# Performance work log

Hardware: AMD Instinct MI355X
Metric: run time of the kernel (lower is better)

Reference implementation:

```python
import jax, jax.numpy as jnp
from jax import lax
import numpy as np

B, T, D_IN = 4, 1024, 8
D_MODEL, N_LAYERS, HORIZON, D_OUT = 512, 2, 24, 8
D_STATE, D_CONV, EXPAND = 64, 4, 2
D_INNER = EXPAND * D_MODEL
DT_RANK = -(-D_MODEL // 16)  # ceil(d_model/16) = 32
LN_EPS = 1e-5


def setup_inputs() -> dict:
    key = jax.random.key(0)
    ks = iter(jax.random.split(key, 24))
    rn = lambda shape, s: jax.random.normal(next(ks), shape, jnp.float32) * s
    A_log = jnp.tile(jnp.log(jnp.arange(1, D_STATE + 1, dtype=jnp.float32)), (N_LAYERS, D_INNER, 1))
    return {
        "x": rn((B, T, D_IN), 1.0),
        "W_in": rn((D_IN, D_MODEL), 0.3), "b_in": jnp.zeros((D_MODEL,), jnp.float32),
        "W_xz": rn((N_LAYERS, D_MODEL, 2 * D_INNER), 0.04),
        "conv_w": rn((N_LAYERS, D_INNER, D_CONV), 0.3), "conv_b": jnp.zeros((N_LAYERS, D_INNER), jnp.float32),
        "W_xproj": rn((N_LAYERS, D_INNER, DT_RANK + 2 * D_STATE), 0.03),
        "W_dt": rn((N_LAYERS, DT_RANK, D_INNER), 0.1), "b_dt": rn((N_LAYERS, D_INNER), 0.1) - 4.0,
        "A_log": A_log, "D_skip": jnp.ones((N_LAYERS, D_INNER), jnp.float32),
        "W_out": rn((N_LAYERS, D_INNER, D_MODEL), 0.03),
        "ln_g": jnp.ones((D_MODEL,), jnp.float32), "ln_b": jnp.zeros((D_MODEL,), jnp.float32),
        "W_h1": rn((D_MODEL, D_MODEL), 0.04), "b_h1": jnp.zeros((D_MODEL,), jnp.float32),
        "W_h2": rn((D_MODEL, HORIZON * D_OUT), 0.04), "b_h2": jnp.zeros((HORIZON * D_OUT,), jnp.float32),
    }


def mamba_block(h, Wxz, cw, cb, Wxp, Wdt, bdt, Alog, Dsk, Wout):
    # h: [B,T,d_model] -> [B,T,d_model]  (mamba-ssm Mamba block, no residual)
    xz = h @ Wxz                                   # [B,T,2*d_inner]
    xb, z = jnp.split(xz, 2, axis=-1)
    # depthwise causal conv over time
    xc = jnp.transpose(xb, (0, 2, 1))              # [B,d_inner,T]
    xc = lax.conv_general_dilated(xc, cw[:, None, :], (1,), [(D_CONV - 1, 0)],
                                  feature_group_count=D_INNER)
    xc = jax.nn.silu(xc + cb[None, :, None])
    xc = jnp.transpose(xc, (0, 2, 1))              # [B,T,d_inner]
    # input-dependent dt, B, C
    xdb = xc @ Wxp                                 # [B,T,dt_rank+2*d_state]
    dt_r = xdb[..., :DT_RANK]
    Bc = xdb[..., DT_RANK:DT_RANK + D_STATE]
    Cc = xdb[..., DT_RANK + D_STATE:]
    dt = jax.nn.softplus(dt_r @ Wdt + bdt)         # [B,T,d_inner]
    A = -jnp.exp(Alog)                             # [d_inner,d_state]

    def step(hst, ins):
        dt_t, B_t, C_t, x_t = ins                  # [B,d_inner],[B,N],[B,N],[B,d_inner]
        dA = jnp.exp(dt_t[..., None] * A)          # [B,d_inner,N]
        hst = dA * hst + dt_t[..., None] * B_t[:, None, :] * x_t[..., None]
        y = jnp.einsum('bdn,bn->bd', hst, C_t)
        return hst, y

    h0 = jnp.zeros((h.shape[0], D_INNER, D_STATE), h.dtype)
    xs = (jnp.transpose(dt, (1, 0, 2)), jnp.transpose(Bc, (1, 0, 2)),
          jnp.transpose(Cc, (1, 0, 2)), jnp.transpose(xc, (1, 0, 2)))
    _, ys = lax.scan(step, h0, xs)                 # ys: [T,B,d_inner]
    y = jnp.transpose(ys, (1, 0, 2)) + Dsk * xc
    y = y * jax.nn.silu(z)
    return y @ Wout


def reference(x, W_in, b_in, W_xz, conv_w, conv_b, W_xproj, W_dt, b_dt, A_log, D_skip,
              W_out, ln_g, ln_b, W_h1, b_h1, W_h2, b_h2):
    h = x @ W_in + b_in                            # [B,T,d_model]
    for i in range(N_LAYERS):
        h = mamba_block(h, W_xz[i], conv_w[i], conv_b[i], W_xproj[i], W_dt[i],
                        b_dt[i], A_log[i], D_skip[i], W_out[i])
    mu = jnp.mean(h, axis=-1, keepdims=True)
    var = jnp.mean(jnp.square(h - mu), axis=-1, keepdims=True)
    h = (h - mu) * lax.rsqrt(var + LN_EPS) * ln_g + ln_b
    last = h[:, -1, :]                             # [B,d_model]
    hid = jax.nn.gelu(last @ W_h1 + b_h1, approximate=False)
    yhat = hid @ W_h2 + b_h2                       # [B,horizon*d_out]
    return yhat.reshape(x.shape[0], HORIZON, D_OUT)
```

## Files before the change

### kernel.cpp

```cpp
#include <hip/hip_runtime.h>
#include <hip/hip_bf16.h>

static constexpr int kB      = 4;
static constexpr int kT      = 1024;
static constexpr int kDIN    = 8;
static constexpr int kDMODEL = 512;
static constexpr int kNLAYER = 2;
static constexpr int kHOR    = 24;
static constexpr int kDOUT   = 8;
static constexpr int kDSTATE = 64;
static constexpr int kDINNER = 1024;
static constexpr int kDTRANK = 32;
static constexpr int kXPROJ  = 160;
static constexpr int kXPAD   = 256;
static constexpr int kBT     = kB * kT;

typedef __bf16 bf16x8 __attribute__((ext_vector_type(8)));
typedef float  f32x4  __attribute__((ext_vector_type(4)));

__device__ __forceinline__ float silu_f(float x)     { return x / (1.f + __expf(-x)); }
__device__ __forceinline__ float softplus_f(float x) { return (x > 20.f) ? x : log1pf(__expf(x)); }
__device__ __forceinline__ float gelu_f(float x)     { return 0.5f * x * (1.f + erff(x * 0.70710678118654752f)); }

__device__ __forceinline__ void gld_lds16(const void* g, void* l) {
    __builtin_amdgcn_global_load_lds(
        (const __attribute__((address_space(1))) unsigned int*)g,
        (__attribute__((address_space(3))) unsigned int*)l, 16, 0, 0);
}

template<int CTRL>
__device__ __forceinline__ float dpp_mov(float v) {
    return __int_as_float(__builtin_amdgcn_update_dpp(
        0, __float_as_int(v), CTRL, 0xf, 0xf, false));
}

__global__ __launch_bounds__(256) void wtrans_kernel(
    const float* __restrict__ in, int K, int N, int in_lstride,
    __hip_bfloat16* __restrict__ out, int Kpad, int out_lstride)
{
    __shared__ float tile[32][33];
    const int tid = threadIdx.x;
    const int n0 = blockIdx.x * 32;
    const int k0 = blockIdx.y * 32;
    const float* inl = in + (size_t)blockIdx.z * in_lstride;
    __hip_bfloat16* outl = out + (size_t)blockIdx.z * out_lstride;

#pragma unroll
    for (int p = 0; p < 4; ++p) {
        int idx = p * 256 + tid;
        int ki = idx >> 5, ni = idx & 31;
        float v = 0.f;
        if (k0 + ki < K && n0 + ni < N) v = inl[(size_t)(k0 + ki) * N + n0 + ni];
        tile[ki][ni] = v;
    }
    __syncthreads();
#pragma unroll
    for (int p = 0; p < 4; ++p) {
        int idx = p * 256 + tid;
        int ni = idx >> 5, ki = idx & 31;
        outl[(size_t)(n0 + ni) * Kpad + k0 + ki] = __float2bfloat16(tile[ki][ni]);
    }
}

template<int MODE, int BN>
__global__ __launch_bounds__(256) void mfma_gemm_bt(
    const __hip_bfloat16* __restrict__ A, int lda,
    const __hip_bfloat16* __restrict__ BT, int ldb,
    const float* __restrict__ bias,
    float* __restrict__ C, int ldc,
    void* __restrict__ C2,
    int K)
{
    __shared__ __align__(16) __hip_bfloat16 sA[128][64];
    __shared__ __align__(16) __hip_bfloat16 sB[BN][64];

    const int tid  = threadIdx.x;
    const int lane = tid & 63;
    const int w    = tid >> 6;
    const int m0   = blockIdx.y * 128;
    const int n0   = blockIdx.x * BN;

    constexpr int NI = 4;
    constexpr int NJ = (BN == 128) ? 4 : 4;
    constexpr int MI = (BN == 128) ? 4 : 2;

    const int wm = (BN == 128) ? (w >> 1) : w;
    const int wn = (BN == 128) ? (w & 1) : 0;
    const int wmrows = (BN == 128) ? 64 : 32;

    f32x4 acc[MI][NJ] = {};

    const int lrow = lane & 15;
    const int lk   = (lane >> 4) << 3;

    const int grow = tid >> 3;
    const int gcol = (tid & 7) * 8;
    char* ldsA = (char*)&sA[0][0] + w * 1024;
    char* ldsB = (char*)&sB[0][0] + w * 1024;

    for (int k0 = 0; k0 < K; k0 += 64) {
        __syncthreads();
#pragma unroll
        for (int p = 0; p < 4; ++p)
            gld_lds16(A + (size_t)(m0 + grow + p * 32) * lda + k0 + gcol, ldsA + p * 4096);
#pragma unroll
        for (int p = 0; p < BN / 32; ++p)
            gld_lds16(BT + (size_t)(n0 + grow + p * 32) * ldb + k0 + gcol, ldsB + p * 4096);
        __syncthreads();
#pragma unroll
        for (int ks = 0; ks < 2; ++ks) {
            bf16x8 af[MI], bfr[NJ];
#pragma unroll
            for (int i = 0; i < MI; ++i)
                af[i] = *reinterpret_cast<const bf16x8*>(&sA[wm * wmrows + i * 16 + lrow][ks * 32 + lk]);
#pragma unroll
            for (int j = 0; j < NJ; ++j)
                bfr[j] = *reinterpret_cast<const bf16x8*>(&sB[wn * 64 + j * 16 + lrow][ks * 32 + lk]);
#pragma unroll
            for (int i = 0; i < MI; ++i)
#pragma unroll
                for (int j = 0; j < NJ; ++j)
                    acc[i][j] = __builtin_amdgcn_mfma_f32_16x16x32_bf16(af[i], bfr[j], acc[i][j], 0, 0, 0);
        }
    }

    const int crow = (lane >> 4) * 4;
    const int ccol = lane & 15;
#pragma unroll
    for (int i = 0; i < MI; ++i) {
#pragma unroll
        for (int j = 0; j < NJ; ++j) {
#pragma unroll
            for (int r = 0; r < 4; ++r) {
                int row = m0 + wm * wmrows + i * 16 + crow + r;
                int col = n0 + wn * 64 + j * 16 + ccol;
                float v = acc[i][j][r];
                if (MODE == 1) {
                    C[(size_t)row * ldc + col] = v;
                    ((__hip_bfloat16*)C2)[(size_t)row * ldc + col] = __float2bfloat16(v);
                } else if (MODE == 2) {
                    float dtv = softplus_f(v + bias[col]);
                    float xcv = __bfloat162float(((const __hip_bfloat16*)C2)[(size_t)row * kDINNER + col]);
                    size_t base = (size_t)(row >> 1) * 4096 + col * 4 + (row & 1) * 2;
                    C[base]     = dtv;
                    C[base + 1] = dtv * xcv;
                } else if (MODE == 4) {
                    if (col < kDINNER)
                        ((__hip_bfloat16*)C)[(size_t)row * ldc + col] = __float2bfloat16(v);
                    else
                        ((__hip_bfloat16*)C2)[(size_t)row * ldc + (col - kDINNER)] =
                            __float2bfloat16(silu_f(v));
                } else {
                    if (col < kDTRANK)
                        ((__hip_bfloat16*)C2)[(size_t)row * kXPAD + col] = __float2bfloat16(v);
                    else if (col < kDTRANK + kDSTATE)
                        C[(size_t)(row >> 1) * 256 + (col - kDTRANK) * 4 + (row & 1) * 2] = v;
                    else if (col < kXPROJ)
                        C[(size_t)(row >> 1) * 256 + (col - kDTRANK - kDSTATE) * 4 + (row & 1) * 2 + 1] = v;
                }
            }
        }
    }
}

__global__ __launch_bounds__(256) void in_proj_kernel(
    const float* __restrict__ x, const float* __restrict__ W,
    const float* __restrict__ b,
    float* __restrict__ h, __hip_bfloat16* __restrict__ hb)
{
    int idx = blockIdx.x * 256 + threadIdx.x;
    int n4 = (idx & 127) * 4;
    int m  = idx >> 7;
    float4 acc = *reinterpret_cast<const float4*>(b + n4);
    const float* xr = x + m * kDIN;
#pragma unroll
    for (int k = 0; k < kDIN; ++k) {
        float4 wv = *reinterpret_cast<const float4*>(W + k * kDMODEL + n4);
        float xv = xr[k];
        acc.x = fmaf(xv, wv.x, acc.x);
        acc.y = fmaf(xv, wv.y, acc.y);
        acc.z = fmaf(xv, wv.z, acc.z);
        acc.w = fmaf(xv, wv.w, acc.w);
    }
    *reinterpret_cast<float4*>(h + (size_t)m * kDMODEL + n4) = acc;
    __bf16 o4[4] = {(__bf16)acc.x, (__bf16)acc.y, (__bf16)acc.z, (__bf16)acc.w};
    *reinterpret_cast<ushort4*>(hb + (size_t)m * kDMODEL + n4) =
        *reinterpret_cast<ushort4*>(o4);
}

__global__ __launch_bounds__(256) void conv_silu_kernel(
    const __hip_bfloat16* __restrict__ xb,
    const float* __restrict__ cw, const float* __restrict__ cb,
    __hip_bfloat16* __restrict__ xc)
{
    int idx = blockIdx.x * 256 + threadIdx.x;
    int dg  = (idx & 127) * 8;
    int bt  = idx >> 7;
    int t   = bt & (kT - 1);

    float4 wv[8];
#pragma unroll
    for (int k = 0; k < 8; ++k)
        wv[k] = *reinterpret_cast<const float4*>(cw + (dg + k) * 4);

    float acc[8];
#pragma unroll
    for (int k = 0; k < 8; ++k) acc[k] = cb[dg + k];

    const __hip_bfloat16* base = xb + (size_t)bt * kDINNER + dg;
    {
        bf16x8 v = *reinterpret_cast<const bf16x8*>(base);
#pragma unroll
        for (int k = 0; k < 8; ++k) acc[k] = fmaf((float)v[k], wv[k].w, acc[k]);
    }
    if (t >= 1) {
        bf16x8 v = *reinterpret_cast<const bf16x8*>(base - kDINNER);
#pragma unroll
        for (int k = 0; k < 8; ++k) acc[k] = fmaf((float)v[k], wv[k].z, acc[k]);
    }
    if (t >= 2) {
        bf16x8 v = *reinterpret_cast<const bf16x8*>(base - 2 * kDINNER);
#pragma unroll
        for (int k = 0; k < 8; ++k) acc[k] = fmaf((float)v[k], wv[k].y, acc[k]);
    }
    if (t >= 3) {
        bf16x8 v = *reinterpret_cast<const bf16x8*>(base - 3 * kDINNER);
#pragma unroll
        for (int k = 0; k < 8; ++k) acc[k] = fmaf((float)v[k], wv[k].x, acc[k]);
    }
    bf16x8 o;
#pragma unroll
    for (int k = 0; k < 8; ++k) o[k] = (__bf16)silu_f(acc[k]);
    *reinterpret_cast<bf16x8*>(xc + (size_t)bt * kDINNER + dg) = o;
}

__global__ __launch_bounds__(256, 4) void scan_kernel(
    const float* __restrict__ dtp,
    const float* __restrict__ xdbi,
    const __hip_bfloat16* __restrict__ xc,
    const __hip_bfloat16* __restrict__ zs,
    const float* __restrict__ Alog,
    const float* __restrict__ Dsk,
    __hip_bfloat16* __restrict__ yg)
{
    __shared__ __align__(16) float sBC[2][16][64][4];
    __shared__ __align__(16) float sDT[2][16][4][4];

    const int tid  = threadIdx.x;
    const int lane = tid & 63;
    const int w    = tid >> 6;
    const int bb = blockIdx.x;
    const int b  = (bb & 7) >> 1;
    const int d0 = ((bb >> 3) + (bb & 1) * 128) * 4;
    const int d  = d0 + w;

    const float a2  = -__expf(Alog[d * kDSTATE + lane]) * 1.44269504f;
    const float dsk = Dsk[d];
    const size_t rowbase  = (size_t)b * kT;
    const size_t pairbase = (size_t)b * (kT / 2);
    float s = 0.f;

    auto stageBC = [&](int c, int buf) {
        const float* src = xdbi + (pairbase + c * 16 + 4 * w) * 256 + lane * 4;
#pragma unroll
        for (int p = 0; p < 4; ++p)
            gld_lds16(src + p * 256, &sBC[buf][4 * w + p][0][0]);
    };
    auto stageDT = [&](int c, int buf) {
        if (w == 0)
            gld_lds16(dtp + (pairbase + c * 16 + (lane >> 2)) * 4096 + (d0 + (lane & 3)) * 4,
                      &sDT[buf][0][0][0]);
    };
    auto loadEP = [&](int c, float& oxv, float& ozv) {
        size_t g = (rowbase + c * 32 + (lane & 31)) * kDINNER + d;
        oxv = (float)((const __bf16*)xc)[g];
        ozv = (float)((const __bf16*)zs)[g];
    };

    float exv = 0.f, ezv = 0.f;
    stageBC(0, 0);
    stageDT(0, 0);
    loadEP(0, exv, ezv);
    __syncthreads();

    for (int c = 0; c < kT / 32; ++c) {
        const int buf = c & 1;
        float nxv = 0.f, nzv = 0.f;
        const bool more = (c + 1 < kT / 32);
        if (more) {
            stageBC(c + 1, buf ^ 1);
            stageDT(c + 1, buf ^ 1);
            loadEP(c + 1, nxv, nzv);
        }

        float yv[32];
#pragma unroll
        for (int p = 0; p < 16; ++p) {
            float4 bc = *reinterpret_cast<const float4*>(&sBC[buf][p][lane][0]);
            float4 dd = *reinterpret_cast<const float4*>(&sDT[buf][p][w][0]);
            float dA0 = exp2f(dd.x * a2);
            s = fmaf(dA0, s, dd.y * bc.x);
            yv[2 * p] = s * bc.y;
            float dA1 = exp2f(dd.z * a2);
            s = fmaf(dA1, s, dd.w * bc.z);
            yv[2 * p + 1] = s * bc.w;
        }

#pragma unroll
        for (int m = 0; m < 16; ++m) {
            float av = yv[2 * m], bv = yv[2 * m + 1];
            float cv = (lane & 1) ? bv : av;
            float dv = (lane & 1) ? av : bv;
            yv[m] = cv + dpp_mov<0xB1>(dv);
        }
#pragma unroll
        for (int m = 0; m < 8; ++m) {
            float av = yv[2 * m], bv = yv[2 * m + 1];
            float cv = (lane & 2) ? bv : av;
            float dv = (lane & 2) ? av : bv;
            yv[m] = cv + dpp_mov<0x4E>(dv);
        }
#pragma unroll
        for (int j = 2; j < 5; ++j) {
            const int S = 1 << j;
#pragma unroll
            for (int m = 0; m < (32 >> (j + 1)); ++m) {
                float av = yv[2 * m], bv = yv[2 * m + 1];
                float cv = (lane & S) ? bv : av;
                float dv = (lane & S) ? av : bv;
                yv[m] = cv + __shfl_xor(dv, S, 64);
            }
        }
        float y = yv[0];
        y += __shfl_xor(y, 32, 64);

        float yo = fmaf(dsk, exv, y) * ezv;
        if (lane < 32) {
            size_t g = (rowbase + c * 32 + lane) * kDINNER + d;
            yg[g] = __float2bfloat16(yo);
        }
        __syncthreads();
        exv = nxv; ezv = nzv;
    }
}

__global__ __launch_bounds__(256) void ln_head_kernel(
    const float* __restrict__ h,
    const float* __restrict__ g, const float* __restrict__ be,
    const float* __restrict__ W1, const float* __restrict__ b1,
    const float* __restrict__ W2, const float* __restrict__ b2,
    float* __restrict__ out)
{
    __shared__ float sln[512];
    __shared__ float shid[512];
    __shared__ float sbuf[8];
    const int b = blockIdx.x, tid = threadIdx.x;
    const float* row = h + (size_t)(b * kT + (kT - 1)) * kDMODEL;

    float v0 = row[tid], v1 = row[tid + 256];
    float s = v0 + v1;
    float q = v0 * v0 + v1 * v1;
#pragma unroll
    for (int m = 32; m >= 1; m >>= 1) {
        s += __shfl_xor(s, m, 64);
        q += __shfl_xor(q, m, 64);
    }
    int wid = tid >> 6;
    if ((tid & 63) == 0) { sbuf[wid] = s; sbuf[4 + wid] = q; }
    __syncthreads();
    if (tid == 0) {
        float S = 0.f, Q = 0.f;
        for (int i = 0; i < 4; ++i) { S += sbuf[i]; Q += sbuf[4 + i]; }
        sbuf[0] = S; sbuf[4] = Q;
    }
    __syncthreads();
    float mean = sbuf[0] * (1.f / kDMODEL);
    float var  = sbuf[4] * (1.f / kDMODEL) - mean * mean;
    float inv  = rsqrtf(var + 1e-5f);
    sln[tid]       = (v0 - mean) * inv * g[tid]       + be[tid];
    sln[tid + 256] = (v1 - mean) * inv * g[tid + 256] + be[tid + 256];
    __syncthreads();

    float a0 = b1[tid], a1 = b1[tid + 256];
#pragma unroll 8
    for (int k = 0; k < kDMODEL; ++k) {
        float lv = sln[k];
        a0 = fmaf(lv, W1[(size_t)k * kDMODEL + tid],       a0);
        a1 = fmaf(lv, W1[(size_t)k * kDMODEL + tid + 256], a1);
    }
    shid[tid]       = gelu_f(a0);
    shid[tid + 256] = gelu_f(a1);
    __syncthreads();

    if (tid < kHOR * kDOUT) {
        float acc = b2[tid];
#pragma unroll 8
        for (int k = 0; k < kDMODEL; ++k)
            acc = fmaf(shid[k], W2[(size_t)k * (kHOR * kDOUT) + tid], acc);
        out[b * (kHOR * kDOUT) + tid] = acc;
    }
}

extern "C" void kernel_launch(void* const* d_in, const int* in_sizes, int n_in,
                              void* d_out, int out_size, void* d_ws, size_t ws_size,
                              hipStream_t stream)
{
    const float* x      = (const float*)d_in[0];
    const float* W_in   = (const float*)d_in[1];
    const float* b_in   = (const float*)d_in[2];
    const float* W_xz   = (const float*)d_in[3];
    const float* conv_w = (const float*)d_in[4];
    const float* conv_b = (const float*)d_in[5];
    const float* W_xp   = (const float*)d_in[6];
    const float* W_dt   = (const float*)d_in[7];
    const float* b_dt   = (const float*)d_in[8];
    const float* A_log  = (const float*)d_in[9];
    const float* D_skip = (const float*)d_in[10];
    const float* W_out  = (const float*)d_in[11];
    const float* ln_g   = (const float*)d_in[12];
    const float* ln_b   = (const float*)d_in[13];
    const float* W_h1   = (const float*)d_in[14];
    const float* b_h1   = (const float*)d_in[15];
    const float* W_h2   = (const float*)d_in[16];
    const float* b_h2   = (const float*)d_in[17];
    float* out = (float*)d_out;

    char* p = (char*)d_ws;
    auto alloc = [&](size_t bytes) { char* q = p; p += (bytes + 255) & ~(size_t)255; return q; };
    float*          h       = (float*)         alloc((size_t)kBT * kDMODEL * 4);
    __hip_bfloat16* h_bf    = (__hip_bfloat16*)alloc((size_t)kBT * kDMODEL * 2);
    __hip_bfloat16* xb_bf   = (__hip_bfloat16*)alloc((size_t)kBT * kDINNER * 2);
    __hip_bfloat16* z_bf    = (__hip_bfloat16*)alloc((size_t)kBT * kDINNER * 2);
    __hip_bfloat16* xc_bf   = (__hip_bfloat16*)alloc((size_t)kBT * kDINNER * 2);
    float*          xdbi    = (float*)         alloc((size_t)(kBT / 2) * 256 * 4);
    __hip_bfloat16* xdb_bf  = (__hip_bfloat16*)alloc((size_t)kBT * kXPAD * 2);
    float*          dtp     = (float*)         alloc((size_t)(kBT / 2) * 4096 * 4);
    __hip_bfloat16* ys_bf   = (__hip_bfloat16*)alloc((size_t)kBT * kDINNER * 2);
    __hip_bfloat16* wxz_bt  = (__hip_bfloat16*)alloc((size_t)2 * 2048 * 512 * 2);
    __hip_bfloat16* wxp_bt  = (__hip_bfloat16*)alloc((size_t)2 * 256 * 1024 * 2);
    __hip_bfloat16* wdt_bt  = (__hip_bfloat16*)alloc((size_t)2 * 1024 * 64 * 2);
    __hip_bfloat16* wout_bt = (__hip_bfloat16*)alloc((size_t)2 * 512 * 1024 * 2);

    wtrans_kernel<<<dim3(64, 16, 2), 256, 0, stream>>>(W_xz, 512,  2048, 512 * 2048, wxz_bt,  512,  2048 * 512);
    wtrans_kernel<<<dim3(8,  32, 2), 256, 0, stream>>>(W_xp, 1024, 160,  1024 * 160, wxp_bt,  1024, 256 * 1024);
    wtrans_kernel<<<dim3(32, 2,  2), 256, 0, stream>>>(W_dt, 32,   1024, 32 * 1024,  wdt_bt,  64,   1024 * 64);
    wtrans_kernel<<<dim3(16, 32, 2), 256, 0, stream>>>(W_out, 1024, 512, 1024 * 512, wout_bt, 1024, 512 * 1024);

    in_proj_kernel<<<(kBT * 128) / 256, 256, 0, stream>>>(x, W_in, b_in, h, h_bf);

    for (int l = 0; l < kNLAYER; ++l) {
        const float* cw_l  = conv_w + (size_t)l * kDINNER * 4;
        const float* cb_l  = conv_b + (size_t)l * kDINNER;
        const float* bdt_l = b_dt   + (size_t)l * kDINNER;
        const float* Al_l  = A_log  + (size_t)l * kDINNER * kDSTATE;
        const float* Dsk_l = D_skip + (size_t)l * kDINNER;
        const __hip_bfloat16* wxz_l  = wxz_bt  + (size_t)l * 2048 * 512;
        const __hip_bfloat16* wxp_l  = wxp_bt  + (size_t)l * 256 * 1024;
        const __hip_bfloat16* wdt_l  = wdt_bt  + (size_t)l * 1024 * 64;
        const __hip_bfloat16* wout_l = wout_bt + (size_t)l * 512 * 1024;

        mfma_gemm_bt<4, 128><<<dim3(16, 32), 256, 0, stream>>>(
            h_bf, kDMODEL, wxz_l, 512, nullptr, (float*)xb_bf, kDINNER, z_bf, kDMODEL);
        conv_silu_kernel<<<(kBT * 128) / 256, 256, 0, stream>>>(xb_bf, cw_l, cb_l, xc_bf);
        mfma_gemm_bt<5, 128><<<dim3(2, 32), 256, 0, stream>>>(
            xc_bf, kDINNER, wxp_l, 1024, nullptr, xdbi, 0, xdb_bf, kDINNER);
        mfma_gemm_bt<2, 128><<<dim3(8, 32), 256, 0, stream>>>(
            xdb_bf, kXPAD, wdt_l, 64, bdt_l, dtp, 0, (void*)xc_bf, 64);
        scan_kernel<<<kB * kDINNER / 4, 256, 0, stream>>>(
            dtp, xdbi, xc_bf, z_bf, Al_l, Dsk_l, ys_bf);
        mfma_gemm_bt<1, 64><<<dim3(8, 32), 256, 0, stream>>>(
            ys_bf, kDINNER, wout_l, 1024, nullptr, h, kDMODEL, h_bf, kDINNER);
    }

    ln_head_kernel<<<kB, 256, 0, stream>>>(h, ln_g, ln_b, W_h1, b_h1, W_h2, b_h2, out);
}
```

Before: 521.2 us.

## Merge weight transposes, move dt*x product into scan, retile x_proj GEMM

Replaces the four weight-transpose launches with a single kernel that dispatches on block index. The dt GEMM epilogue now writes plain row-major softplus(dt) and no longer builds the interleaved dt/dt*x buffer. The scan kernel instead loads dt and xc directly, forms dt*x itself and writes it to LDS through registers after the compute phase. Compute is wrapped in s_setprio, and the x_proj GEMM uses BN=64 with three column blocks. The aim is to shrink the dt buffer traffic and the launch count, at the cost of extra global loads inside the scan loop.

```diff
diff --git a/kernel.cpp b/kernel.cpp
--- a/kernel.cpp
+++ b/kernel.cpp
@@ -5,7 +5,6 @@
 static constexpr int kT      = 1024;
 static constexpr int kDIN    = 8;
 static constexpr int kDMODEL = 512;
-static constexpr int kNLAYER = 2;
 static constexpr int kHOR    = 24;
 static constexpr int kDOUT   = 8;
 static constexpr int kDSTATE = 64;
@@ -14,6 +13,7 @@
 static constexpr int kXPROJ  = 160;
 static constexpr int kXPAD   = 256;
 static constexpr int kBT     = kB * kT;
+static constexpr int kNLAYER = 2;
 
 typedef __bf16 bf16x8 __attribute__((ext_vector_type(8)));
 typedef float  f32x4  __attribute__((ext_vector_type(4)));
@@ -34,23 +34,44 @@
         0, __float_as_int(v), CTRL, 0xf, 0xf, false));
 }
 
-__global__ __launch_bounds__(256) void wtrans_kernel(
-    const float* __restrict__ in, int K, int N, int in_lstride,
-    __hip_bfloat16* __restrict__ out, int Kpad, int out_lstride)
+__global__ __launch_bounds__(256) void wtrans_all_kernel(
+    const float* __restrict__ Wxz, const float* __restrict__ Wxp,
+    const float* __restrict__ Wdt, const float* __restrict__ Wout,
+    __hip_bfloat16* __restrict__ oxz, __hip_bfloat16* __restrict__ oxp,
+    __hip_bfloat16* __restrict__ odt, __hip_bfloat16* __restrict__ oout)
 {
     __shared__ float tile[32][33];
+    const int bid = blockIdx.x;
     const int tid = threadIdx.x;
-    const int n0 = blockIdx.x * 32;
-    const int k0 = blockIdx.y * 32;
-    const float* inl = in + (size_t)blockIdx.z * in_lstride;
-    __hip_bfloat16* outl = out + (size_t)blockIdx.z * out_lstride;
+
+    const float* in; __hip_bfloat16* out;
+    int K, N, Kpad, TX, loc;
+    if (bid < 2048) {
+        int l = bid >> 10; loc = bid & 1023;
+        in = Wxz + (size_t)l * 512 * 2048; out = oxz + (size_t)l * 2048 * 512;
+        K = 512; N = 2048; Kpad = 512; TX = 64;
+    } else if (bid < 2368) {
+        int r = bid - 2048; int l = r / 160; loc = r % 160;
+        in = Wxp + (size_t)l * 1024 * 160; out = oxp + (size_t)l * 256 * 1024;
+        K = 1024; N = 160; Kpad = 1024; TX = 5;
+    } else if (bid < 2496) {
+        int r = bid - 2368; int l = r >> 6; loc = r & 63;
+        in = Wdt + (size_t)l * 32 * 1024; out = odt + (size_t)l * 1024 * 64;
+        K = 32; N = 1024; Kpad = 64; TX = 32;
+    } else {
+        int r = bid - 2496; int l = r >> 9; loc = r & 511;
+        in = Wout + (size_t)l * 1024 * 512; out = oout + (size_t)l * 512 * 1024;
+        K = 1024; N = 512; Kpad = 1024; TX = 16;
+    }
+    const int n0 = (loc % TX) * 32;
+    const int k0 = (loc / TX) * 32;
 
 #pragma unroll
     for (int p = 0; p < 4; ++p) {
         int idx = p * 256 + tid;
         int ki = idx >> 5, ni = idx & 31;
         float v = 0.f;
-        if (k0 + ki < K && n0 + ni < N) v = inl[(size_t)(k0 + ki) * N + n0 + ni];
+        if (k0 + ki < K && n0 + ni < N) v = in[(size_t)(k0 + ki) * N + n0 + ni];
         tile[ki][ni] = v;
     }
     __syncthreads();
@@ -58,7 +79,8 @@
     for (int p = 0; p < 4; ++p) {
         int idx = p * 256 + tid;
         int ni = idx >> 5, ki = idx & 31;
-        outl[(size_t)(n0 + ni) * Kpad + k0 + ki] = __float2bfloat16(tile[ki][ni]);
+        if (n0 + ni < N)
+            out[(size_t)(n0 + ni) * Kpad + k0 + ki] = __float2bfloat16(tile[ki][ni]);
     }
 }
 
@@ -80,10 +102,8 @@
     const int m0   = blockIdx.y * 128;
     const int n0   = blockIdx.x * BN;
 
-    constexpr int NI = 4;
-    constexpr int NJ = (BN == 128) ? 4 : 4;
+    constexpr int NJ = 4;
     constexpr int MI = (BN == 128) ? 4 : 2;
-
     const int wm = (BN == 128) ? (w >> 1) : w;
     const int wn = (BN == 128) ? (w & 1) : 0;
     const int wmrows = (BN == 128) ? 64 : 32;
@@ -139,11 +159,7 @@
                     C[(size_t)row * ldc + col] = v;
                     ((__hip_bfloat16*)C2)[(size_t)row * ldc + col] = __float2bfloat16(v);
                 } else if (MODE == 2) {
-                    float dtv = softplus_f(v + bias[col]);
-                    float xcv = __bfloat162float(((const __hip_bfloat16*)C2)[(size_t)row * kDINNER + col]);
-                    size_t base = (size_t)(row >> 1) * 4096 + col * 4 + (row & 1) * 2;
-                    C[base]     = dtv;
-                    C[base + 1] = dtv * xcv;
+                    C[(size_t)row * ldc + col] = softplus_f(v + bias[col]);
                 } else if (MODE == 4) {
                     if (col < kDINNER)
                         ((__hip_bfloat16*)C)[(size_t)row * ldc + col] = __float2bfloat16(v);
@@ -235,7 +251,7 @@
 }
 
 __global__ __launch_bounds__(256, 4) void scan_kernel(
-    const float* __restrict__ dtp,
+    const float* __restrict__ dt,
     const float* __restrict__ xdbi,
     const __hip_bfloat16* __restrict__ xc,
     const __hip_bfloat16* __restrict__ zs,
@@ -266,10 +282,19 @@
         for (int p = 0; p < 4; ++p)
             gld_lds16(src + p * 256, &sBC[buf][4 * w + p][0][0]);
     };
-    auto stageDT = [&](int c, int buf) {
-        if (w == 0)
-            gld_lds16(dtp + (pairbase + c * 16 + (lane >> 2)) * 4096 + (d0 + (lane & 3)) * 4,
-                      &sDT[buf][0][0][0]);
+    const int lp = tid >> 3, lw = (tid >> 1) & 3, lst = tid & 1;
+    auto loadDT = [&](int c, float& odt, float& odx) {
+        if (tid < 128) {
+            size_t g = (rowbase + c * 32 + lp * 2 + lst) * kDINNER + d0 + lw;
+            odt = dt[g];
+            odx = odt * (float)((const __bf16*)xc)[g];
+        }
+    };
+    auto writeDT = [&](int buf, float vdt, float vdx) {
+        if (tid < 128) {
+            sDT[buf][lp][lw][lst * 2]     = vdt;
+            sDT[buf][lp][lw][lst * 2 + 1] = vdx;
+        }
     };
     auto loadEP = [&](int c, float& oxv, float& ozv) {
         size_t g = (rowbase + c * 32 + (lane & 31)) * kDINNER + d;
@@ -277,22 +302,24 @@
         ozv = (float)((const __bf16*)zs)[g];
     };
 
-    float exv = 0.f, ezv = 0.f;
+    float pdt = 0.f, pdx = 0.f, exv = 0.f, ezv = 0.f;
     stageBC(0, 0);
-    stageDT(0, 0);
+    loadDT(0, pdt, pdx);
     loadEP(0, exv, ezv);
+    writeDT(0, pdt, pdx);
     __syncthreads();
 
     for (int c = 0; c < kT / 32; ++c) {
         const int buf = c & 1;
-        float nxv = 0.f, nzv = 0.f;
+        float ndt = 0.f, ndx = 0.f, nxv = 0.f, nzv = 0.f;
         const bool more = (c + 1 < kT / 32);
         if (more) {
             stageBC(c + 1, buf ^ 1);
-            stageDT(c + 1, buf ^ 1);
+            loadDT(c + 1, ndt, ndx);
             loadEP(c + 1, nxv, nzv);
         }
 
+        __builtin_amdgcn_s_setprio(1);
         float yv[32];
 #pragma unroll
         for (int p = 0; p < 16; ++p) {
@@ -333,12 +360,14 @@
         }
         float y = yv[0];
         y += __shfl_xor(y, 32, 64);
+        __builtin_amdgcn_s_setprio(0);
 
         float yo = fmaf(dsk, exv, y) * ezv;
         if (lane < 32) {
             size_t g = (rowbase + c * 32 + lane) * kDINNER + d;
             yg[g] = __float2bfloat16(yo);
         }
+        if (more) writeDT(buf ^ 1, ndt, ndx);
         __syncthreads();
         exv = nxv; ezv = nzv;
     }
@@ -434,17 +463,15 @@
     __hip_bfloat16* xc_bf   = (__hip_bfloat16*)alloc((size_t)kBT * kDINNER * 2);
     float*          xdbi    = (float*)         alloc((size_t)(kBT / 2) * 256 * 4);
     __hip_bfloat16* xdb_bf  = (__hip_bfloat16*)alloc((size_t)kBT * kXPAD * 2);
-    float*          dtp     = (float*)         alloc((size_t)(kBT / 2) * 4096 * 4);
+    float*          dtb     = (float*)         alloc((size_t)kBT * kDINNER * 4);
     __hip_bfloat16* ys_bf   = (__hip_bfloat16*)alloc((size_t)kBT * kDINNER * 2);
     __hip_bfloat16* wxz_bt  = (__hip_bfloat16*)alloc((size_t)2 * 2048 * 512 * 2);
     __hip_bfloat16* wxp_bt  = (__hip_bfloat16*)alloc((size_t)2 * 256 * 1024 * 2);
     __hip_bfloat16* wdt_bt  = (__hip_bfloat16*)alloc((size_t)2 * 1024 * 64 * 2);
     __hip_bfloat16* wout_bt = (__hip_bfloat16*)alloc((size_t)2 * 512 * 1024 * 2);
 
-    wtrans_kernel<<<dim3(64, 16, 2), 256, 0, stream>>>(W_xz, 512,  2048, 512 * 2048, wxz_bt,  512,  2048 * 512);
-    wtrans_kernel<<<dim3(8,  32, 2), 256, 0, stream>>>(W_xp, 1024, 160,  1024 * 160, wxp_bt,  1024, 256 * 1024);
-    wtrans_kernel<<<dim3(32, 2,  2), 256, 0, stream>>>(W_dt, 32,   1024, 32 * 1024,  wdt_bt,  64,   1024 * 64);
-    wtrans_kernel<<<dim3(16, 32, 2), 256, 0, stream>>>(W_out, 1024, 512, 1024 * 512, wout_bt, 1024, 512 * 1024);
+    wtrans_all_kernel<<<3520, 256, 0, stream>>>(
+        W_xz, W_xp, W_dt, W_out, wxz_bt, wxp_bt, wdt_bt, wout_bt);
 
     in_proj_kernel<<<(kBT * 128) / 256, 256, 0, stream>>>(x, W_in, b_in, h, h_bf);
 
@@ -462,12 +489,12 @@
         mfma_gemm_bt<4, 128><<<dim3(16, 32), 256, 0, stream>>>(
             h_bf, kDMODEL, wxz_l, 512, nullptr, (float*)xb_bf, kDINNER, z_bf, kDMODEL);
         conv_silu_kernel<<<(kBT * 128) / 256, 256, 0, stream>>>(xb_bf, cw_l, cb_l, xc_bf);
-        mfma_gemm_bt<5, 128><<<dim3(2, 32), 256, 0, stream>>>(
+        mfma_gemm_bt<5, 64><<<dim3(3, 32), 256, 0, stream>>>(
             xc_bf, kDINNER, wxp_l, 1024, nullptr, xdbi, 0, xdb_bf, kDINNER);
         mfma_gemm_bt<2, 128><<<dim3(8, 32), 256, 0, stream>>>(
-            xdb_bf, kXPAD, wdt_l, 64, bdt_l, dtp, 0, (void*)xc_bf, 64);
+            xdb_bf, kXPAD, wdt_l, 64, bdt_l, dtb, kDINNER, nullptr, 64);
         scan_kernel<<<kB * kDINNER / 4, 256, 0, stream>>>(
-            dtp, xdbi, xc_bf, z_bf, Al_l, Dsk_l, ys_bf);
+            dtb, xdbi, xc_bf, z_bf, Al_l, Dsk_l, ys_bf);
         mfma_gemm_bt<1, 64><<<dim3(8, 32), 256, 0, stream>>>(
             ys_bf, kDINNER, wout_l, 1024, nullptr, h, kDMODEL, h_bf, kDINNER);
     }
```

Measured after the change: 487.1 us. -6.5%, faster.
